# Kernel optimization log

Hardware: AMD Instinct MI355X
Metric: run time of the kernel (lower is better)

The kernel has to match this reference:

```python
import jax, jax.numpy as jnp
import numpy as np

N_NODES = 100000
N_EDGES = 3200000
D_IN = 128
HEADS = 8
F_OUT = 64


def setup_inputs() -> dict:
    key = jax.random.key(0)
    k1, k2, k3, k4, k5, k6 = jax.random.split(key, 6)
    node_features = jax.random.normal(k1, (N_NODES, D_IN), dtype=jnp.float32)
    linear_proj = jax.random.normal(k2, (D_IN, HEADS * F_OUT), dtype=jnp.float32) * (1.0 / np.sqrt(D_IN))
    scoring_fn_source = jax.random.normal(k3, (1, HEADS, F_OUT), dtype=jnp.float32) * 0.1
    scoring_fn_target = jax.random.normal(k4, (1, HEADS, F_OUT), dtype=jnp.float32) * 0.1
    edge_index = jax.random.randint(k5, (2, N_EDGES), 0, N_NODES, dtype=jnp.int64)
    return {
        'node_features': node_features,
        'linear_proj': linear_proj,
        'scoring_fn_source': scoring_fn_source,
        'scoring_fn_target': scoring_fn_target,
        'edge_index': edge_index,
    }


def reference(node_features, linear_proj, scoring_fn_source, scoring_fn_target, edge_index):
    # node_features: [N, D_in]; edge_index: [2, E] (row 0 = src, row 1 = trg)
    N = node_features.shape[0]
    H, F = scoring_fn_source.shape[1], scoring_fn_source.shape[2]

    # linear projection: [N, H, F]
    proj = (node_features @ linear_proj).reshape(N, H, F)

    # per-node attention scores: [N, H]
    scores_source = jnp.sum(proj * scoring_fn_source, axis=-1)
    scores_target = jnp.sum(proj * scoring_fn_target, axis=-1)

    src, trg = edge_index[0], edge_index[1]
    # lift to edges + LeakyReLU: [E, H]
    scores_per_edge = jax.nn.leaky_relu(scores_source[src] + scores_target[trg],
                                        negative_slope=0.2)

    # neighborhood-aware softmax over edges sharing the same target node
    seg_max = jax.ops.segment_max(scores_per_edge, trg, num_segments=N)   # [N, H]
    exp_scores = jnp.exp(scores_per_edge - seg_max[trg])                  # [E, H]
    seg_sum = jax.ops.segment_sum(exp_scores, trg, num_segments=N)        # [N, H]
    attentions_per_edge = exp_scores / (seg_sum[trg] + 1e-16)             # [E, H]
    return attentions_per_edge
```

## Files before the change

### kernel.cpp

```cpp
#include <hip/hip_runtime.h>
#include <hip/hip_fp16.h>

#define D_IN   128
#define HEADS  8
#define FOUT   64
#define NOUT   16
#define NPB    512
#define NPB_SH 9
#define NB_MAX 1024
#define CHUNK  8192
#define NBLK_MAX 1024
#define TPN    8
#define SROWS  64
#define SPAD   129
#define DET_BLOCKS 128

typedef unsigned __attribute__((ext_vector_type(2))) uint2v;
typedef float    __attribute__((ext_vector_type(4))) float4v;

__device__ __forceinline__ unsigned pack2(float a, float b) {
    union { __half2 h; unsigned u; } c;
    c.h = __floats2half2_rn(a, b);
    return c.u;
}
__device__ __forceinline__ float2 up2(unsigned u) {
    union { unsigned x; __half2 h; } c;
    c.x = u;
    return __half22float2(c.h);
}

__device__ __forceinline__ unsigned ntl_u(const unsigned* p) {
    return __builtin_nontemporal_load(p);
}
__device__ __forceinline__ uint2v ntl_u2(const unsigned* p) {
    return __builtin_nontemporal_load((const uint2v*)p);
}
__device__ __forceinline__ float4v ntl_f4(const float* p) {
    return __builtin_nontemporal_load((const float4v*)p);
}
__device__ __forceinline__ void nts_f4(float* p, float4v v) {
    __builtin_nontemporal_store(v, (float4v*)p);
}

__device__ __forceinline__ void load_edge(const unsigned int* idx, int e, int E,
                                          bool is64, unsigned int& s, unsigned int& t) {
    if (is64) {
        uint2v a = ntl_u2(idx + 2 * (size_t)e);
        uint2v b = ntl_u2(idx + 2 * ((size_t)E + e));
        s = a.x; t = b.x;
    } else {
        s = ntl_u(idx + e);
        t = ntl_u(idx + (size_t)E + e);
    }
}

__global__ void k_fold_w(const float* __restrict__ W,
                         const float* __restrict__ a_src,
                         const float* __restrict__ a_trg,
                         float* __restrict__ Wc,
                         unsigned int* __restrict__ flag,
                         int* __restrict__ binTotal, int NB) {
    int t = blockIdx.x * blockDim.x + threadIdx.x;
    if (t == 0) flag[0] = 0u;
    if (binTotal && t < NB) binTotal[t] = 0;
    if (t >= D_IN * HEADS) return;
    int d = t >> 3, h = t & 7;
    const float* wrow = W + d * (HEADS * FOUT) + h * FOUT;
    float s1 = 0.f, s2 = 0.f;
    #pragma unroll 4
    for (int f = 0; f < FOUT; ++f) {
        float w = wrow[f];
        s1 += w * a_src[h * FOUT + f];
        s2 += w * a_trg[h * FOUT + f];
    }
    Wc[h * D_IN + d]           = s1;
    Wc[(HEADS + h) * D_IN + d] = s2;
}

__global__ void k_scores_h(const float* __restrict__ x,
                           const float* __restrict__ Wc,
                           float* __restrict__ strg_f,
                           __half* __restrict__ ssrc_h, int N,
                           const unsigned int* __restrict__ idx, int E,
                           int dwords, unsigned int* __restrict__ flag,
                           int* __restrict__ histB, int NB, int NBLK,
                           int* __restrict__ binTotal) {
    int tid = threadIdx.x;

    if ((int)blockIdx.x < DET_BLOCKS) {
        unsigned int local = 0;
        int stride = DET_BLOCKS * 256;
        for (int i = blockIdx.x * 256 + tid; 2 * i + 1 < dwords; i += stride)
            local |= idx[2 * i + 1];
        if (__any(local != 0) && (tid & 63) == 0)
            atomicOr(flag, 1u);
    }

    if ((int)blockIdx.x < NBLK) {
        __shared__ int h[NB_MAX];
        __shared__ int s_i32;
        if (tid == 0) s_i32 = 0;
        for (int i = tid; i < NB; i += blockDim.x) h[i] = 0;
        __syncthreads();
        if (tid < 64) {
            unsigned int v = (2 * tid + 1 < 2 * E) ? idx[2 * tid + 1] : 0u;
            if (__any(v != 0) && tid == 0) s_i32 = 1;
        }
        __syncthreads();
        bool is64 = (s_i32 == 0);

        int base = blockIdx.x * CHUNK;
        int lim  = min(base + CHUNK, E);
        for (int e = base + tid; e < lim; e += blockDim.x) {
            unsigned int t = is64 ? ntl_u2(idx + 2 * ((size_t)E + e)).x
                                  : ntl_u(idx + (size_t)E + e);
            atomicAdd(&h[t >> NPB_SH], 1);
        }
        __syncthreads();
        for (int i = tid; i < NB; i += blockDim.x) {
            histB[(size_t)i * NBLK + blockIdx.x] = h[i];
            if (h[i]) atomicAdd(&binTotal[i], h[i]);
        }
        __syncthreads();
    }

    __shared__ float xt[SROWS * SPAD];
    int node0 = blockIdx.x * SROWS;
    int nrows = min(SROWS, N - node0);
    if (nrows <= 0) return;

    for (int i = tid; i < nrows * 32; i += 256) {
        int r = i >> 5, c = (i & 31) * 4;
        float4v v = ntl_f4(x + (size_t)(node0 + r) * D_IN + c);
        float* dst = &xt[r * SPAD + c];
        dst[0] = v.x; dst[1] = v.y; dst[2] = v.z; dst[3] = v.w;
    }
    __syncthreads();

    int r  = tid & 63;
    int og = tid >> 6;
    if (r >= nrows) return;
    int n = node0 + r;

    const float* w = Wc + og * 4 * D_IN;
    float a0 = 0.f, a1 = 0.f, a2 = 0.f, a3 = 0.f;
    const float* xr = &xt[r * SPAD];
    #pragma unroll 8
    for (int d = 0; d < D_IN; ++d) {
        float xv = xr[d];
        a0 += xv * w[d];
        a1 += xv * w[D_IN + d];
        a2 += xv * w[2 * D_IN + d];
        a3 += xv * w[3 * D_IN + d];
    }

    if (og < 2) {
        uint2 hp;
        hp.x = pack2(a0, a1);
        hp.y = pack2(a2, a3);
        *(uint2*)(ssrc_h + (size_t)n * HEADS + og * 4) = hp;
    } else {
        *(float4*)(strg_f + (size_t)n * HEADS + (og - 2) * 4) =
            make_float4(a0, a1, a2, a3);
    }
}

__global__ void k_scan(const int* __restrict__ histB,
                       int* __restrict__ histA, int NB, int NBLK,
                       const int* __restrict__ binTotal,
                       int* __restrict__ binBase) {
    int b = blockIdx.x;
    int tid = threadIdx.x;
    if (b < NB) {
        __shared__ int v[NBLK_MAX];
        v[tid] = (tid < NBLK) ? histB[(size_t)b * NBLK + tid] : 0;
        __syncthreads();
        int w = 1; while (w < NBLK) w <<= 1;
        for (int off = 1; off < w; off <<= 1) {
            int t = (tid >= off) ? v[tid - off] : 0;
            __syncthreads();
            v[tid] += t;
            __syncthreads();
        }
        if (tid < NBLK)
            histA[(size_t)tid * NB + b] = tid ? v[tid - 1] : 0;
    } else {
        __shared__ int v2[NB_MAX];
        v2[tid] = (tid < NB) ? binTotal[tid] : 0;
        __syncthreads();
        int w = 1; while (w < NB) w <<= 1;
        for (int off = 1; off < w; off <<= 1) {
            int t = (tid >= off) ? v2[tid - off] : 0;
            __syncthreads();
            v2[tid] += t;
            __syncthreads();
        }
        if (tid < NB)
            binBase[tid] = tid ? v2[tid - 1] : 0;
    }
}

__global__ void k_scatter(const unsigned int* __restrict__ idx, int E,
                          const unsigned int* __restrict__ flag,
                          const int* __restrict__ histA, int NB,
                          const int* __restrict__ binBase,
                          unsigned int* __restrict__ binned) {
    __shared__ int cnt[NB_MAX];
    for (int i = threadIdx.x; i < NB; i += blockDim.x)
        cnt[i] = binBase[i] + histA[(size_t)blockIdx.x * NB + i];
    __syncthreads();
    bool is64 = (*flag == 0u);
    int base = blockIdx.x * CHUNK;
    int lim  = min(base + CHUNK, E);
    for (int e = base + threadIdx.x; e < lim; e += blockDim.x) {
        unsigned int s, t;
        load_edge(idx, e, E, is64, s, t);
        int pos = atomicAdd(&cnt[t >> NPB_SH], 1);
        binned[pos] = s | ((t & (NPB - 1u)) << 20);
    }
}

__global__ void k_sort2(const unsigned int* __restrict__ binned,
                        const int* __restrict__ binBase,
                        const int* __restrict__ binTotal,
                        unsigned int* __restrict__ sortedSrc,
                        int* __restrict__ rowPtr, int N, int NB) {
    __shared__ int cnt[NPB];
    __shared__ int scn[NPB];
    int b = blockIdx.x;
    int node0 = b << NPB_SH;
    int start = binBase[b], total = binTotal[b];
    int i = threadIdx.x;
    int T = blockDim.x;

    if (i < NPB) cnt[i] = 0;
    __syncthreads();
    for (int e = i; e < total; e += T)
        atomicAdd(&cnt[binned[start + e] >> 20], 1);
    __syncthreads();

    if (i < NPB) scn[i] = cnt[i];
    __syncthreads();
    for (int o = 1; o < NPB; o <<= 1) {
        int t = (i < NPB && i >= o) ? scn[i - o] : 0;
        __syncthreads();
        if (i < NPB) scn[i] += t;
        __syncthreads();
    }
    if (i < NPB) {
        int excl = scn[i] - cnt[i];
        cnt[i] = excl;
        int n = node0 + i;
        if (n < N) rowPtr[n] = start + excl;
    }
    if (b == NB - 1 && i == 0) rowPtr[N] = start + total;
    __syncthreads();

    for (int e = i; e < total; e += T) {
        unsigned int v = binned[start + e];
        int pos = atomicAdd(&cnt[v >> 20], 1);
        sortedSrc[start + pos] = v & 0xFFFFFu;
    }
}

__global__ void k_nodesum(const unsigned int* __restrict__ sortedSrc,
                          const int* __restrict__ rowPtr,
                          const __half* __restrict__ ssrc_h,
                          const float* __restrict__ strg_f,
                          __half* __restrict__ combo, int N) {
    int gt = blockIdx.x * blockDim.x + threadIdx.x;
    int n  = gt >> 3;
    int k  = gt & (TPN - 1);
    if (n >= N) return;

    int r0 = rowPtr[n], r1 = rowPtr[n + 1];
    const float4* tp = (const float4*)(strg_f + (size_t)n * HEADS);
    float4 ta = tp[0], tb = tp[1];
    float st[8] = { ta.x, ta.y, ta.z, ta.w, tb.x, tb.y, tb.z, tb.w };
    float acc[8] = { 0, 0, 0, 0, 0, 0, 0, 0 };

    for (int e = r0 + k; e < r1; e += TPN) {
        unsigned int s = sortedSrc[e];
        uint4 sv = *(const uint4*)(ssrc_h + (size_t)s * HEADS);
        float2 f01 = up2(sv.x), f23 = up2(sv.y), f45 = up2(sv.z), f67 = up2(sv.w);
        float vs[8] = { f01.x, f01.y, f23.x, f23.y, f45.x, f45.y, f67.x, f67.y };
        #pragma unroll
        for (int h = 0; h < HEADS; ++h) {
            float sc = vs[h] + st[h];
            sc = sc > 0.f ? sc : 0.2f * sc;
            acc[h] += expf(sc);
        }
    }
    #pragma unroll
    for (int h = 0; h < HEADS; ++h) {
        acc[h] += __shfl_xor(acc[h], 1, 64);
        acc[h] += __shfl_xor(acc[h], 2, 64);
        acc[h] += __shfl_xor(acc[h], 4, 64);
    }
    if (k == 0) {
        float rs[8];
        #pragma unroll
        for (int h = 0; h < HEADS; ++h) rs[h] = 1.0f / (acc[h] + 1e-16f);
        uint4 c0, c1;
        c0.x = pack2(st[0], st[1]);  c0.y = pack2(st[2], st[3]);
        c0.z = pack2(st[4], st[5]);  c0.w = pack2(st[6], st[7]);
        c1.x = pack2(rs[0], rs[1]);  c1.y = pack2(rs[2], rs[3]);
        c1.z = pack2(rs[4], rs[5]);  c1.w = pack2(rs[6], rs[7]);
        uint4* cp = (uint4*)(combo + (size_t)n * 16);
        cp[0] = c0;
        cp[1] = c1;
    }
}

__device__ __forceinline__ void edge_out_one(unsigned int s, unsigned int t,
                                             const __half* __restrict__ ssrc_h,
                                             const __half* __restrict__ combo,
                                             float* o) {
    uint4 sv = *(const uint4*)(ssrc_h + (size_t)s * HEADS);
    const uint4* cp = (const uint4*)(combo + (size_t)t * 16);
    uint4 c0 = cp[0], c1 = cp[1];
    float2 s01 = up2(sv.x), s23 = up2(sv.y), s45 = up2(sv.z), s67 = up2(sv.w);
    float2 t01 = up2(c0.x), t23 = up2(c0.y), t45 = up2(c0.z), t67 = up2(c0.w);
    float2 r01 = up2(c1.x), r23 = up2(c1.y), r45 = up2(c1.z), r67 = up2(c1.w);
    float ss[8] = { s01.x, s01.y, s23.x, s23.y, s45.x, s45.y, s67.x, s67.y };
    float st[8] = { t01.x, t01.y, t23.x, t23.y, t45.x, t45.y, t67.x, t67.y };
    float rs[8] = { r01.x, r01.y, r23.x, r23.y, r45.x, r45.y, r67.x, r67.y };
    #pragma unroll
    for (int h = 0; h < HEADS; ++h) {
        float sc = ss[h] + st[h];
        sc = sc > 0.f ? sc : 0.2f * sc;
        o[h] = expf(sc) * rs[h];
    }
}

__global__ void k_edge_out_c(const unsigned int* __restrict__ idx, int E,
                             const __half* __restrict__ ssrc_h,
                             const __half* __restrict__ combo,
                             const unsigned int* __restrict__ flag,
                             float* __restrict__ out) {
    int base = blockIdx.x * 512;
    int t    = threadIdx.x;
    int e0 = base + t;
    int e1 = base + t + 256;
    if (e0 >= E) return;
    bool is64 = (*flag == 0u);
    bool v1 = e1 < E;

    unsigned int s0, t0, s1, t1;
    load_edge(idx, e0, E, is64, s0, t0);
    int e1c = v1 ? e1 : e0;
    load_edge(idx, e1c, E, is64, s1, t1);

    float o0[8], o1[8];
    edge_out_one(s0, t0, ssrc_h, combo, o0);
    edge_out_one(s1, t1, ssrc_h, combo, o1);

    float4v a0 = { o0[0], o0[1], o0[2], o0[3] };
    float4v a1 = { o0[4], o0[5], o0[6], o0[7] };
    nts_f4(out + (size_t)e0 * HEADS,     a0);
    nts_f4(out + (size_t)e0 * HEADS + 4, a1);
    if (v1) {
        float4v b0 = { o1[0], o1[1], o1[2], o1[3] };
        float4v b1 = { o1[4], o1[5], o1[6], o1[7] };
        nts_f4(out + (size_t)e1 * HEADS,     b0);
        nts_f4(out + (size_t)e1 * HEADS + 4, b1);
    }
}

__device__ __forceinline__ void edge_scores(const float* ssrc, const float* strg,
                                            unsigned int s, unsigned int t, float* ex) {
    const float4* sp = (const float4*)(ssrc + (size_t)s * HEADS);
    const float4* tp = (const float4*)(strg + (size_t)t * HEADS);
    float4 sa = sp[0], sb = sp[1], ta = tp[0], tb = tp[1];
    float v[8] = { sa.x + ta.x, sa.y + ta.y, sa.z + ta.z, sa.w + ta.w,
                   sb.x + tb.x, sb.y + tb.y, sb.z + tb.z, sb.w + tb.w };
    #pragma unroll
    for (int h = 0; h < HEADS; ++h) {
        float sc = v[h];
        sc = sc > 0.f ? sc : 0.2f * sc;
        ex[h] = expf(sc);
    }
}

__global__ void k_detect_fb(const unsigned int* __restrict__ idx_w, int nwords,
                            unsigned int* __restrict__ flag) {
    unsigned int local = 0;
    int stride = gridDim.x * blockDim.x;
    for (int i = blockIdx.x * blockDim.x + threadIdx.x; 2 * i + 1 < nwords; i += stride)
        local |= idx_w[2 * i + 1];
    if (__any(local != 0) && (threadIdx.x & 63) == 0)
        atomicOr(flag, 1u);
}

__global__ void k_scores_fb(const float* __restrict__ x,
                            const float* __restrict__ Wc,
                            float* __restrict__ ssrc_f,
                            float* __restrict__ strg_f, int N) {
    __shared__ float xt[SROWS * SPAD];
    int node0 = blockIdx.x * SROWS;
    int tid   = threadIdx.x;
    int nrows = min(SROWS, N - node0);

    for (int i = tid; i < nrows * 32; i += 256) {
        int r = i >> 5, c = (i & 31) * 4;
        float4v v = ntl_f4(x + (size_t)(node0 + r) * D_IN + c);
        float* dst = &xt[r * SPAD + c];
        dst[0] = v.x; dst[1] = v.y; dst[2] = v.z; dst[3] = v.w;
    }
    __syncthreads();

    int r  = tid & 63;
    int og = tid >> 6;
    if (r >= nrows) return;
    int n = node0 + r;

    const float* w = Wc + og * 4 * D_IN;
    float a0 = 0.f, a1 = 0.f, a2 = 0.f, a3 = 0.f;
    const float* xr = &xt[r * SPAD];
    #pragma unroll 8
    for (int d = 0; d < D_IN; ++d) {
        float xv = xr[d];
        a0 += xv * w[d];
        a1 += xv * w[D_IN + d];
        a2 += xv * w[2 * D_IN + d];
        a3 += xv * w[3 * D_IN + d];
    }
    float4 res = make_float4(a0, a1, a2, a3);
    if (og < 2) *(float4*)(ssrc_f + (size_t)n * HEADS + og * 4)       = res;
    else        *(float4*)(strg_f + (size_t)n * HEADS + (og - 2) * 4) = res;
}

__global__ void k_edge_sum(const unsigned int* __restrict__ idx, int E,
                           const float* __restrict__ ssrc,
                           const float* __restrict__ strg,
                           float* __restrict__ sums,
                           const unsigned int* __restrict__ flag) {
    int e = blockIdx.x * blockDim.x + threadIdx.x;
    if (e >= E) return;
    bool is64 = (*flag == 0u);
    unsigned int s, t;
    load_edge(idx, e, E, is64, s, t);
    float ex[8];
    edge_scores(ssrc, strg, s, t, ex);
    float* dst = sums + (size_t)t * HEADS;
    #pragma unroll
    for (int h = 0; h < HEADS; ++h)
        atomicAdd(dst + h, ex[h]);
}

__global__ void k_edge_out(const unsigned int* __restrict__ idx, int E,
                           const float* __restrict__ ssrc,
                           const float* __restrict__ strg,
                           const float* __restrict__ sums,
                           const unsigned int* __restrict__ flag,
                           float* __restrict__ out) {
    int e = blockIdx.x * blockDim.x + threadIdx.x;
    if (e >= E) return;
    bool is64 = (*flag == 0u);
    unsigned int s, t;
    load_edge(idx, e, E, is64, s, t);
    float ex[8];
    edge_scores(ssrc, strg, s, t, ex);
    const float4* sm = (const float4*)(sums + (size_t)t * HEADS);
    float4 m0 = sm[0], m1 = sm[1];
    float4 o0, o1;
    o0.x = ex[0] / (m0.x + 1e-16f);  o0.y = ex[1] / (m0.y + 1e-16f);
    o0.z = ex[2] / (m0.z + 1e-16f);  o0.w = ex[3] / (m0.w + 1e-16f);
    o1.x = ex[4] / (m1.x + 1e-16f);  o1.y = ex[5] / (m1.y + 1e-16f);
    o1.z = ex[6] / (m1.z + 1e-16f);  o1.w = ex[7] / (m1.w + 1e-16f);
    float4* op = (float4*)(out + (size_t)e * HEADS);
    op[0] = o0;
    op[1] = o1;
}

extern "C" void kernel_launch(void* const* d_in, const int* in_sizes, int n_in,
                              void* d_out, int out_size, void* d_ws, size_t ws_size,
                              hipStream_t stream) {
    const float*        x     = (const float*)d_in[0];
    const float*        W     = (const float*)d_in[1];
    const float*        a_src = (const float*)d_in[2];
    const float*        a_trg = (const float*)d_in[3];
    const unsigned int* idx   = (const unsigned int*)d_in[4];

    const int N  = in_sizes[0] / D_IN;
    const int E  = in_sizes[4] / 2;
    const int NH = N * HEADS;
    const int NB   = (N + NPB - 1) / NPB;
    const int NBLK = (E + CHUNK - 1) / CHUNK;

    float* out = (float*)d_out;
    char*  ws  = (char*)d_ws;
    size_t NHb = (size_t)NH * sizeof(float);

    size_t off = 0;
    auto alloc = [&](size_t bytes) { size_t o = off; off = (off + bytes + 255) & ~(size_t)255; return o; };
    unsigned int* flag     = (unsigned int*)(ws + alloc(8));
    float*        strg_f   = (float*)(ws + alloc(NHb));
    __half*       ssrc_h   = (__half*)(ws + alloc((size_t)NH * sizeof(__half)));
    __half*       combo    = (__half*)(ws + alloc((size_t)N * 16 * sizeof(__half)));
    float*        Wc       = (float*)(ws + alloc(NOUT * D_IN * sizeof(float)));
    int*          histA    = (int*)(ws + alloc((size_t)NBLK * NB * sizeof(int)));
    int*          histB    = (int*)(ws + alloc((size_t)NB * NBLK * sizeof(int)));
    int*          binTotal = (int*)(ws + alloc((size_t)NB * sizeof(int)));
    int*          binBase  = (int*)(ws + alloc((size_t)NB * sizeof(int)));
    unsigned int* binned   = (unsigned int*)(ws + alloc((size_t)E * sizeof(unsigned int)));
    unsigned int* sortedS  = (unsigned int*)(ws + alloc((size_t)E * sizeof(unsigned int)));
    int*          rowPtr   = (int*)(ws + alloc((size_t)(N + 1) * sizeof(int)));

    const bool fast = (off <= ws_size) && (NB <= NB_MAX) && (NBLK <= NBLK_MAX)
                      && (N < (1 << 20));

    int dwords = in_sizes[4];
    if (dwords > (1 << 20)) dwords = 1 << 20;

    if (fast) {
        k_fold_w <<<(D_IN * HEADS + 255) / 256, 256, 0, stream>>>(W, a_src, a_trg, Wc,
                                                                  flag, binTotal, NB);
        k_scores_h <<<(N + SROWS - 1) / SROWS, 256, 0, stream>>>(x, Wc, strg_f,
                                                                 ssrc_h, N, idx, E,
                                                                 dwords, flag,
                                                                 histB, NB, NBLK,
                                                                 binTotal);
        k_scan    <<<NB + 1, NBLK_MAX, 0, stream>>>(histB, histA, NB, NBLK,
                                                    binTotal, binBase);
        k_scatter <<<NBLK, 512, 0, stream>>>(idx, E, flag, histA, NB, binBase,
                                             binned);
        k_sort2   <<<NB, 1024, 0, stream>>>(binned, binBase, binTotal, sortedS,
                                            rowPtr, N, NB);
        k_nodesum <<<(N * TPN + 511) / 512, 512, 0, stream>>>(sortedS, rowPtr,
                                                              ssrc_h, strg_f,
                                                              combo, N);
        k_edge_out_c <<<(E + 511) / 512, 256, 0, stream>>>(idx, E, ssrc_h, combo,
                                                           flag, out);
    } else {
        size_t o2 = 0;
        auto alloc2 = [&](size_t bytes) { size_t o = o2; o2 = (o2 + bytes + 255) & ~(size_t)255; return o; };
        unsigned int* fb_flag = (unsigned int*)(ws + alloc2(8));
        float*        fb_Wc   = (float*)(ws + alloc2(NOUT * D_IN * sizeof(float)));
        float*        fb_sums = (float*)(ws + alloc2(NHb));
        float*        fb_ssrc = (float*)(ws + alloc2(NHb));
        float*        fb_strg = (float*)(ws + alloc2(NHb));

        hipMemsetAsync(fb_sums, 0, NHb, stream);
        k_fold_w <<<(D_IN * HEADS + 255) / 256, 256, 0, stream>>>(W, a_src, a_trg,
                                                                  fb_Wc, fb_flag,
                                                                  (int*)nullptr, 0);
        k_detect_fb <<<128, 256, 0, stream>>>(idx, dwords, fb_flag);
        k_scores_fb <<<(N + SROWS - 1) / SROWS, 256, 0, stream>>>(x, fb_Wc, fb_ssrc,
                                                                  fb_strg, N);
        int eblocks = (E + 255) / 256;
        k_edge_sum <<<eblocks, 256, 0, stream>>>(idx, E, fb_ssrc, fb_strg, fb_sums,
                                                 fb_flag);
        k_edge_out <<<eblocks, 256, 0, stream>>>(idx, E, fb_ssrc, fb_strg, fb_sums,
                                                 fb_flag, out);
    }
}
```

Baseline: 214.4 us.

## Remove scan kernel by folding prefix sums into scatter and sort

Deletes the separate k_scan launch. Each scatter block now scans bin totals itself and sums the histogram row for its own block offset, and the sort kernel derives its bin base with shared atomics. This saves one launch and the histA and binBase intermediate buffers, but each thread in k_scatter serially reads up to NBLK histogram entries, adding redundant global reads. The edge output kernel is also changed back to one edge per thread. NB_MAX is reduced to 512, which the shared-memory scan assumes.

```diff
diff --git a/kernel.cpp b/kernel.cpp
--- a/kernel.cpp
+++ b/kernel.cpp
@@ -7,7 +7,7 @@
 #define NOUT   16
 #define NPB    512
 #define NPB_SH 9
-#define NB_MAX 1024
+#define NB_MAX 512
 #define CHUNK  8192
 #define NBLK_MAX 1024
 #define TPN    8
@@ -165,54 +165,37 @@
     }
 }
 
-__global__ void k_scan(const int* __restrict__ histB,
-                       int* __restrict__ histA, int NB, int NBLK,
-                       const int* __restrict__ binTotal,
-                       int* __restrict__ binBase) {
-    int b = blockIdx.x;
-    int tid = threadIdx.x;
-    if (b < NB) {
-        __shared__ int v[NBLK_MAX];
-        v[tid] = (tid < NBLK) ? histB[(size_t)b * NBLK + tid] : 0;
-        __syncthreads();
-        int w = 1; while (w < NBLK) w <<= 1;
-        for (int off = 1; off < w; off <<= 1) {
-            int t = (tid >= off) ? v[tid - off] : 0;
-            __syncthreads();
-            v[tid] += t;
-            __syncthreads();
-        }
-        if (tid < NBLK)
-            histA[(size_t)tid * NB + b] = tid ? v[tid - 1] : 0;
-    } else {
-        __shared__ int v2[NB_MAX];
-        v2[tid] = (tid < NB) ? binTotal[tid] : 0;
-        __syncthreads();
-        int w = 1; while (w < NB) w <<= 1;
-        for (int off = 1; off < w; off <<= 1) {
-            int t = (tid >= off) ? v2[tid - off] : 0;
-            __syncthreads();
-            v2[tid] += t;
-            __syncthreads();
-        }
-        if (tid < NB)
-            binBase[tid] = tid ? v2[tid - 1] : 0;
-    }
-}
-
 __global__ void k_scatter(const unsigned int* __restrict__ idx, int E,
                           const unsigned int* __restrict__ flag,
-                          const int* __restrict__ histA, int NB,
-                          const int* __restrict__ binBase,
+                          const int* __restrict__ histB, int NB, int NBLK,
+                          const int* __restrict__ binTotal,
                           unsigned int* __restrict__ binned) {
     __shared__ int cnt[NB_MAX];
-    for (int i = threadIdx.x; i < NB; i += blockDim.x)
-        cnt[i] = binBase[i] + histA[(size_t)blockIdx.x * NB + i];
-    __syncthreads();
+    __shared__ int sc[512];
+    int b   = blockIdx.x;
+    int tid = threadIdx.x;
+
+    sc[tid] = (tid < NB) ? binTotal[tid] : 0;
+    __syncthreads();
+    #pragma unroll
+    for (int off = 1; off < 512; off <<= 1) {
+        int t = (tid >= off) ? sc[tid - off] : 0;
+        __syncthreads();
+        sc[tid] += t;
+        __syncthreads();
+    }
+    if (tid < NB) {
+        int o = 0;
+        const int* row = histB + (size_t)tid * NBLK;
+        for (int j = 0; j < b; ++j) o += row[j];
+        cnt[tid] = (tid ? sc[tid - 1] : 0) + o;
+    }
+    __syncthreads();
+
     bool is64 = (*flag == 0u);
-    int base = blockIdx.x * CHUNK;
+    int base = b * CHUNK;
     int lim  = min(base + CHUNK, E);
-    for (int e = base + threadIdx.x; e < lim; e += blockDim.x) {
+    for (int e = base + tid; e < lim; e += blockDim.x) {
         unsigned int s, t;
         load_edge(idx, e, E, is64, s, t);
         int pos = atomicAdd(&cnt[t >> NPB_SH], 1);
@@ -221,20 +204,25 @@
 }
 
 __global__ void k_sort2(const unsigned int* __restrict__ binned,
-                        const int* __restrict__ binBase,
                         const int* __restrict__ binTotal,
                         unsigned int* __restrict__ sortedSrc,
                         int* __restrict__ rowPtr, int N, int NB) {
     __shared__ int cnt[NPB];
     __shared__ int scn[NPB];
+    __shared__ int s_base;
     int b = blockIdx.x;
     int node0 = b << NPB_SH;
-    int start = binBase[b], total = binTotal[b];
     int i = threadIdx.x;
     int T = blockDim.x;
 
+    if (i == 0) s_base = 0;
     if (i < NPB) cnt[i] = 0;
     __syncthreads();
+    if (i < b) atomicAdd(&s_base, binTotal[i]);
+    __syncthreads();
+    int start = s_base;
+    int total = binTotal[b];
+
     for (int e = i; e < total; e += T)
         atomicAdd(&cnt[binned[start + e] >> 20], 1);
     __syncthreads();
@@ -312,59 +300,40 @@
     }
 }
 
-__device__ __forceinline__ void edge_out_one(unsigned int s, unsigned int t,
-                                             const __half* __restrict__ ssrc_h,
-                                             const __half* __restrict__ combo,
-                                             float* o) {
+__global__ void k_edge_out_c(const unsigned int* __restrict__ idx, int E,
+                             const __half* __restrict__ ssrc_h,
+                             const __half* __restrict__ combo,
+                             const unsigned int* __restrict__ flag,
+                             float* __restrict__ out) {
+    int e = blockIdx.x * blockDim.x + threadIdx.x;
+    if (e >= E) return;
+    bool is64 = (*flag == 0u);
+    unsigned int s, t;
+    load_edge(idx, e, E, is64, s, t);
+
     uint4 sv = *(const uint4*)(ssrc_h + (size_t)s * HEADS);
     const uint4* cp = (const uint4*)(combo + (size_t)t * 16);
     uint4 c0 = cp[0], c1 = cp[1];
+
     float2 s01 = up2(sv.x), s23 = up2(sv.y), s45 = up2(sv.z), s67 = up2(sv.w);
     float2 t01 = up2(c0.x), t23 = up2(c0.y), t45 = up2(c0.z), t67 = up2(c0.w);
     float2 r01 = up2(c1.x), r23 = up2(c1.y), r45 = up2(c1.z), r67 = up2(c1.w);
+
     float ss[8] = { s01.x, s01.y, s23.x, s23.y, s45.x, s45.y, s67.x, s67.y };
     float st[8] = { t01.x, t01.y, t23.x, t23.y, t45.x, t45.y, t67.x, t67.y };
     float rs[8] = { r01.x, r01.y, r23.x, r23.y, r45.x, r45.y, r67.x, r67.y };
+
+    float o[8];
     #pragma unroll
     for (int h = 0; h < HEADS; ++h) {
         float sc = ss[h] + st[h];
         sc = sc > 0.f ? sc : 0.2f * sc;
         o[h] = expf(sc) * rs[h];
     }
-}
-
-__global__ void k_edge_out_c(const unsigned int* __restrict__ idx, int E,
-                             const __half* __restrict__ ssrc_h,
-                             const __half* __restrict__ combo,
-                             const unsigned int* __restrict__ flag,
-                             float* __restrict__ out) {
-    int base = blockIdx.x * 512;
-    int t    = threadIdx.x;
-    int e0 = base + t;
-    int e1 = base + t + 256;
-    if (e0 >= E) return;
-    bool is64 = (*flag == 0u);
-    bool v1 = e1 < E;
-
-    unsigned int s0, t0, s1, t1;
-    load_edge(idx, e0, E, is64, s0, t0);
-    int e1c = v1 ? e1 : e0;
-    load_edge(idx, e1c, E, is64, s1, t1);
-
-    float o0[8], o1[8];
-    edge_out_one(s0, t0, ssrc_h, combo, o0);
-    edge_out_one(s1, t1, ssrc_h, combo, o1);
-
-    float4v a0 = { o0[0], o0[1], o0[2], o0[3] };
-    float4v a1 = { o0[4], o0[5], o0[6], o0[7] };
-    nts_f4(out + (size_t)e0 * HEADS,     a0);
-    nts_f4(out + (size_t)e0 * HEADS + 4, a1);
-    if (v1) {
-        float4v b0 = { o1[0], o1[1], o1[2], o1[3] };
-        float4v b1 = { o1[4], o1[5], o1[6], o1[7] };
-        nts_f4(out + (size_t)e1 * HEADS,     b0);
-        nts_f4(out + (size_t)e1 * HEADS + 4, b1);
-    }
+    float4v o0 = { o[0], o[1], o[2], o[3] };
+    float4v o1 = { o[4], o[5], o[6], o[7] };
+    nts_f4(out + (size_t)e * HEADS,     o0);
+    nts_f4(out + (size_t)e * HEADS + 4, o1);
 }
 
 __device__ __forceinline__ void edge_scores(const float* ssrc, const float* strg,
@@ -499,10 +468,8 @@
     __half*       ssrc_h   = (__half*)(ws + alloc((size_t)NH * sizeof(__half)));
     __half*       combo    = (__half*)(ws + alloc((size_t)N * 16 * sizeof(__half)));
     float*        Wc       = (float*)(ws + alloc(NOUT * D_IN * sizeof(float)));
-    int*          histA    = (int*)(ws + alloc((size_t)NBLK * NB * sizeof(int)));
     int*          histB    = (int*)(ws + alloc((size_t)NB * NBLK * sizeof(int)));
     int*          binTotal = (int*)(ws + alloc((size_t)NB * sizeof(int)));
-    int*          binBase  = (int*)(ws + alloc((size_t)NB * sizeof(int)));
     unsigned int* binned   = (unsigned int*)(ws + alloc((size_t)E * sizeof(unsigned int)));
     unsigned int* sortedS  = (unsigned int*)(ws + alloc((size_t)E * sizeof(unsigned int)));
     int*          rowPtr   = (int*)(ws + alloc((size_t)(N + 1) * sizeof(int)));
@@ -521,16 +488,14 @@
                                                                  dwords, flag,
                                                                  histB, NB, NBLK,
                                                                  binTotal);
-        k_scan    <<<NB + 1, NBLK_MAX, 0, stream>>>(histB, histA, NB, NBLK,
-                                                    binTotal, binBase);
-        k_scatter <<<NBLK, 512, 0, stream>>>(idx, E, flag, histA, NB, binBase,
-                                             binned);
-        k_sort2   <<<NB, 1024, 0, stream>>>(binned, binBase, binTotal, sortedS,
+        k_scatter <<<NBLK, 512, 0, stream>>>(idx, E, flag, histB, NB, NBLK,
+                                             binTotal, binned);
+        k_sort2   <<<NB, 1024, 0, stream>>>(binned, binTotal, sortedS,
                                             rowPtr, N, NB);
         k_nodesum <<<(N * TPN + 511) / 512, 512, 0, stream>>>(sortedS, rowPtr,
                                                               ssrc_h, strg_f,
                                                               combo, N);
-        k_edge_out_c <<<(E + 511) / 512, 256, 0, stream>>>(idx, E, ssrc_h, combo,
+        k_edge_out_c <<<(E + 255) / 256, 256, 0, stream>>>(idx, E, ssrc_h, combo,
                                                            flag, out);
     } else {
         size_t o2 = 0;
```

Result: slower. 246.5 us (+14.9%).
